# Kernel tuning notes

Measured on AMD Instinct MI355X. Metric: run time of the kernel, lower is better.

The kernel has to match this reference:

```python
import jax, jax.numpy as jnp
import numpy as np

N = 100000   # nodes
E = 1600000  # edges (avg degree 16)
D = 128      # in_dim == hidden
L = 3        # num_layers
G = 512      # graphs in batch


def setup_inputs() -> dict:
    key = jax.random.key(0)
    ks = jax.random.split(key, 14)
    s = 0.05
    return {
        "x": jax.random.normal(ks[0], (N, D), jnp.float32),
        "edge_index": jax.random.randint(ks[1], (2, E), 0, N, dtype=jnp.int32),
        "batch": jnp.sort(jax.random.randint(ks[2], (N,), 0, G, dtype=jnp.int32)),
        "W1": jax.random.normal(ks[3], (L, D, D), jnp.float32) * s,
        "b1": jax.random.normal(ks[4], (L, D), jnp.float32) * s,
        "W2": jax.random.normal(ks[5], (L, D, D), jnp.float32) * s,
        "b2": jax.random.normal(ks[6], (L, D), jnp.float32) * s,
        "gamma": jax.random.uniform(ks[7], (L, D), jnp.float32, 0.5, 1.5),
        "beta": jax.random.normal(ks[8], (L, D), jnp.float32) * s,
        "run_mean": jax.random.normal(ks[9], (L, D), jnp.float32) * s,
        "run_var": jax.random.uniform(ks[10], (L, D), jnp.float32, 0.5, 1.5),
        "eps": jnp.zeros((L,), jnp.float32),
        "lin1_W": jax.random.normal(ks[11], (D, D), jnp.float32) * s,
        "lin1_b": jax.random.normal(ks[12], (D,), jnp.float32) * s,
    }


def _bn(h, g, b, m, v):
    # BatchNorm1d in eval mode (running stats)
    return (h - m) * jax.lax.rsqrt(v + 1e-5) * g + b


def reference(x, edge_index, batch, W1, b1, W2, b2, gamma, beta,
              run_mean, run_var, eps, lin1_W, lin1_b):
    n = x.shape[0]
    src, dst = edge_index[0], edge_index[1]
    h = x
    for l in range(L):  # small fixed layer count
        # GINConv: sum-aggregate neighbor features then (1+eps)*self + agg
        agg = jax.ops.segment_sum(h[src], dst, num_segments=n)  # [N, D]
        z = (1.0 + eps[l]) * h + agg
        z = jax.nn.relu(z @ W1[l] + b1[l])
        z = jax.nn.relu(z @ W2[l] + b2[l])
        h = _bn(z, gamma[l], beta[l], run_mean[l], run_var[l])
    # global_mean_pool over graph ids
    counts = jax.ops.segment_sum(jnp.ones((n,), h.dtype), batch, num_segments=G)
    pooled = jax.ops.segment_sum(h, batch, num_segments=G)
    pooled = pooled / jnp.maximum(counts, 1.0)[:, None]  # [G, D]
    # lin1 + ReLU (dropout is identity in eval)
    return jax.nn.relu(pooled @ lin1_W + lin1_b)
```

## Files before the change

kernel.cpp:

```cpp
#include <hip/hip_runtime.h>
#include <hip/hip_bf16.h>

#define NN 100000
#define NE 1600000
#define DD 128
#define NL 3
#define NG 512
#define CSRP (NE + 8 * NN)
#define BSHIFT 9
#define NBUCK2 ((NN + 511) / 512)
#define ABLKS 512
#define ECHUNK (NE / ABLKS)

#define CONV_BLKS 12501
#define PREPW_BLKS 384
#define INIT_BLKS (CONV_BLKS + PREPW_BLKS + 1)

typedef __attribute__((ext_vector_type(8))) short bf16x8;
typedef __attribute__((ext_vector_type(4))) float f32x4;

__device__ __forceinline__ unsigned short f2bf(float f) {
    union { float f; unsigned int u; } x; x.f = f;
    unsigned int r = x.u + 0x7FFFu + ((x.u >> 16) & 1u);
    return (unsigned short)(r >> 16);
}
__device__ __forceinline__ float bf2f(unsigned short u) {
    union { unsigned int u; float f; } x; x.u = ((unsigned int)u) << 16;
    return x.f;
}
__device__ __forceinline__ float bflo(unsigned int v) { return bf2f((unsigned short)(v & 0xffffu)); }
__device__ __forceinline__ float bfhi(unsigned int v) { return bf2f((unsigned short)(v >> 16)); }
__device__ __forceinline__ unsigned cvtpk(float lo, float hi) {
    unsigned r;
    asm("v_cvt_pk_bf16_f32 %0, %1, %2" : "=v"(r) : "v"(lo), "v"(hi));
    return r;
}

__global__ __launch_bounds__(256) void init_all(const float* __restrict__ x,
                                                unsigned short* __restrict__ h0,
                                                unsigned short* __restrict__ h1,
                                                const float* __restrict__ W1,
                                                const float* __restrict__ W2,
                                                unsigned short* __restrict__ wbf,
                                                int* __restrict__ bcnt) {
    int bb = blockIdx.x;
    if (bb < CONV_BLKS) {
        long long t = (long long)bb * 256 + threadIdx.x;
        long long base = t * 4;
        if (base < (long long)NN * DD) {
            float4 v = *reinterpret_cast<const float4*>(x + base);
            ushort4 p;
            p.x = f2bf(v.x); p.y = f2bf(v.y); p.z = f2bf(v.z); p.w = f2bf(v.w);
            *reinterpret_cast<ushort4*>(h0 + base) = p;
        } else if (base < (long long)(NN + 1) * DD) {
            ushort4 z = {0, 0, 0, 0};
            *reinterpret_cast<ushort4*>(h0 + base) = z;
            *reinterpret_cast<ushort4*>(h1 + base) = z;
        }
        return;
    }
    bb -= CONV_BLKS;
    if (bb < PREPW_BLKS) {
        int idx = bb * 256 + threadIdx.x;
        int k = idx & 127;
        int n = (idx >> 7) & 127;
        int w = (idx >> 14) & 1;
        int l = idx >> 15;
        const float* src = w ? W2 : W1;
        wbf[idx] = f2bf(src[(l * DD + k) * DD + n]);
        return;
    }
    int i = threadIdx.x;
    if (i < NBUCK2) bcnt[i] = 0;
}

__global__ __launch_bounds__(256) void bcount(const int* __restrict__ ei,
                                              int* __restrict__ bcnt) {
    __shared__ int hist[NBUCK2];
    int tid = threadIdx.x;
    int e0 = blockIdx.x * ECHUNK;
    for (int i = tid; i < NBUCK2; i += 256) hist[i] = 0;
    __syncthreads();
    for (int i = tid; i < ECHUNK; i += 256)
        atomicAdd(&hist[ei[NE + e0 + i] >> BSHIFT], 1);
    __syncthreads();
    for (int i = tid; i < NBUCK2; i += 256) {
        int h = hist[i];
        if (h) atomicAdd(&bcnt[i], h);
    }
}

__global__ __launch_bounds__(256) void bscan(const int* __restrict__ bcnt,
                                             int* __restrict__ cboff,
                                             int* __restrict__ gpos) {
    __shared__ int s[256];
    int tid = threadIdx.x;
    int sum = (tid < NBUCK2) ? bcnt[tid] : 0;
    s[tid] = sum;
    __syncthreads();
    for (int o = 1; o < 256; o <<= 1) {
        int t = (tid >= o) ? s[tid - o] : 0;
        __syncthreads();
        s[tid] += t;
        __syncthreads();
    }
    if (tid < NBUCK2) {
        cboff[tid] = s[tid] - sum;
        gpos[tid] = 0;
    }
    if (tid == 0) cboff[NBUCK2] = NE;
}

__global__ __launch_bounds__(256) void binA(const int* __restrict__ ei,
                                            const int* __restrict__ cboff,
                                            int* __restrict__ gpos,
                                            int* __restrict__ ebuf) {
    __shared__ int hist[NBUCK2];
    __shared__ int sbase[NBUCK2];
    int tid = threadIdx.x;
    int e0 = blockIdx.x * ECHUNK;
    for (int i = tid; i < NBUCK2; i += 256) hist[i] = 0;
    __syncthreads();
    for (int i = tid; i < ECHUNK; i += 256) {
        int d = ei[NE + e0 + i];
        atomicAdd(&hist[d >> BSHIFT], 1);
    }
    __syncthreads();
    for (int i = tid; i < NBUCK2; i += 256) {
        int h = hist[i];
        sbase[i] = (h > 0) ? atomicAdd(&gpos[i], h) : 0;
        hist[i] = 0;
    }
    __syncthreads();
    for (int i = tid; i < ECHUNK; i += 256) {
        int s2 = ei[e0 + i];
        int d = ei[NE + e0 + i];
        int b = d >> BSHIFT;
        int pos = atomicAdd(&hist[b], 1);
        ebuf[cboff[b] + sbase[b] + pos] = s2 | ((d & 511) << 17);
    }
}

__global__ __launch_bounds__(256) void bpre(const int* __restrict__ ebuf,
                                            const int* __restrict__ cboff,
                                            int* __restrict__ rp,
                                            int* __restrict__ bsum) {
    __shared__ int lcnt[512];
    __shared__ int s[256];
    int b = blockIdx.x;
    int tid = threadIdx.x;
    lcnt[tid] = 0;
    lcnt[tid + 256] = 0;
    __syncthreads();
    int st = cboff[b], en = cboff[b + 1];
    for (int i = st + tid; i < en; i += 256)
        atomicAdd(&lcnt[ebuf[i] >> 17], 1);
    __syncthreads();
    int d0 = (lcnt[2 * tid] + 7) & ~7;
    int d1 = (lcnt[2 * tid + 1] + 7) & ~7;
    int ps = d0 + d1;
    s[tid] = ps;
    __syncthreads();
    for (int o = 1; o < 256; o <<= 1) {
        int t = (tid >= o) ? s[tid - o] : 0;
        __syncthreads();
        s[tid] += t;
        __syncthreads();
    }
    int base = s[tid] - ps;
    int node0 = (b << BSHIFT) + 2 * tid;
    if (node0 < NN) rp[node0] = base;
    if (node0 + 1 < NN) rp[node0 + 1] = base + d0;
    if (tid == 255) bsum[b] = s[255];
}

__global__ __launch_bounds__(256) void bscan2(const int* __restrict__ bsum,
                                              int* __restrict__ bbase,
                                              int* __restrict__ rp) {
    __shared__ int s[256];
    int tid = threadIdx.x;
    int sum = (tid < NBUCK2) ? bsum[tid] : 0;
    s[tid] = sum;
    __syncthreads();
    for (int o = 1; o < 256; o <<= 1) {
        int t = (tid >= o) ? s[tid - o] : 0;
        __syncthreads();
        s[tid] += t;
        __syncthreads();
    }
    if (tid < NBUCK2) bbase[tid] = s[tid] - sum;
    if (tid == 255) rp[NN] = s[255];
}

__global__ __launch_bounds__(256) void binB2(const int* __restrict__ ebuf,
                                             const int* __restrict__ cboff,
                                             const int* __restrict__ bbase,
                                             int* __restrict__ rp,
                                             int* __restrict__ csr) {
    __shared__ int rpl[512];
    __shared__ int lcnt[512];
    int b = blockIdx.x;
    int tid = threadIdx.x;
    int bb = bbase[b];
    for (int i = tid; i < 512; i += 256) {
        int node = (b << BSHIFT) + i;
        int v = 0;
        if (node < NN) {
            v = rp[node] + bb;
            rp[node] = v;
        }
        rpl[i] = v;
        lcnt[i] = 0;
    }
    __syncthreads();
    int st = cboff[b], en = cboff[b + 1];
    for (int i = st + tid; i < en; i += 256) {
        int v = ebuf[i];
        int dl = v >> 17;
        int pos = atomicAdd(&lcnt[dl], 1);
        csr[rpl[dl] + pos] = v & 0x1FFFF;
    }
    __syncthreads();
    for (int i = tid; i < 512; i += 256) {
        int node = (b << BSHIFT) + i;
        if (node >= NN) continue;
        int d = lcnt[i];
        int pd = (d + 7) & ~7;
        int base = rpl[i];
        for (int j = d; j < pd; ++j) csr[base + j] = NN;
    }
}

__global__ __launch_bounds__(256) void layer_fused(
    const unsigned short* __restrict__ hin,
    const int* __restrict__ rp,
    const int* __restrict__ csr,
    const unsigned short* __restrict__ w1t,
    const unsigned short* __restrict__ w2t,
    const float* __restrict__ b1,
    const float* __restrict__ b2,
    const float* __restrict__ gamma,
    const float* __restrict__ beta,
    const float* __restrict__ rmean,
    const float* __restrict__ rvar,
    const float* __restrict__ epsv,
    unsigned short* __restrict__ hout)
{
    __shared__ unsigned short z_lds[16 * 136];
    const int tid = threadIdx.x;
    const int lane = tid & 63;
    const int wave = tid >> 6;
    const int gid = lane >> 4;
    const int lg = lane & 15;
    const int row0 = blockIdx.x * 16;
    const float epl = 1.0f + epsv[0];
    const size_t lgo = (size_t)lg * 8;

#define ACC8(v) do { \
    acc[0] += bflo((v).x); acc[1] += bfhi((v).x); \
    acc[2] += bflo((v).y); acc[3] += bfhi((v).y); \
    acc[4] += bflo((v).z); acc[5] += bfhi((v).z); \
    acc[6] += bflo((v).w); acc[7] += bfhi((v).w); } while (0)

    const int rbase = row0 + (wave << 2);
    int pv = (lane < 5) ? rp[rbase + lane] : 0;
    const int st = __shfl(pv, gid);
    const int en = __shfl(pv, gid + 1);
    const int myrow = rbase + gid;

    float acc[8];
    {
        uint4 sv = *reinterpret_cast<const uint4*>(hin + (size_t)myrow * DD + lgo);
        acc[0] = epl * bflo(sv.x); acc[1] = epl * bfhi(sv.x);
        acc[2] = epl * bflo(sv.y); acc[3] = epl * bfhi(sv.y);
        acc[4] = epl * bflo(sv.z); acc[5] = epl * bfhi(sv.z);
        acc[6] = epl * bflo(sv.w); acc[7] = epl * bfhi(sv.w);
    }
    int c0 = st;
    for (; c0 + 16 <= en; c0 += 16) {
        int4 idA = *reinterpret_cast<const int4*>(csr + c0);
        int4 idB = *reinterpret_cast<const int4*>(csr + c0 + 4);
        int4 idC = *reinterpret_cast<const int4*>(csr + c0 + 8);
        int4 idD = *reinterpret_cast<const int4*>(csr + c0 + 12);
        uint4 v0 = *reinterpret_cast<const uint4*>(hin + (size_t)idA.x * DD + lgo);
        uint4 v1 = *reinterpret_cast<const uint4*>(hin + (size_t)idA.y * DD + lgo);
        uint4 v2 = *reinterpret_cast<const uint4*>(hin + (size_t)idA.z * DD + lgo);
        uint4 v3 = *reinterpret_cast<const uint4*>(hin + (size_t)idA.w * DD + lgo);
        uint4 v4 = *reinterpret_cast<const uint4*>(hin + (size_t)idB.x * DD + lgo);
        uint4 v5 = *reinterpret_cast<const uint4*>(hin + (size_t)idB.y * DD + lgo);
        uint4 v6 = *reinterpret_cast<const uint4*>(hin + (size_t)idB.z * DD + lgo);
        uint4 v7 = *reinterpret_cast<const uint4*>(hin + (size_t)idB.w * DD + lgo);
        uint4 v8 = *reinterpret_cast<const uint4*>(hin + (size_t)idC.x * DD + lgo);
        uint4 v9 = *reinterpret_cast<const uint4*>(hin + (size_t)idC.y * DD + lgo);
        uint4 va = *reinterpret_cast<const uint4*>(hin + (size_t)idC.z * DD + lgo);
        uint4 vb = *reinterpret_cast<const uint4*>(hin + (size_t)idC.w * DD + lgo);
        uint4 vc = *reinterpret_cast<const uint4*>(hin + (size_t)idD.x * DD + lgo);
        uint4 vd = *reinterpret_cast<const uint4*>(hin + (size_t)idD.y * DD + lgo);
        uint4 ve = *reinterpret_cast<const uint4*>(hin + (size_t)idD.z * DD + lgo);
        uint4 vf = *reinterpret_cast<const uint4*>(hin + (size_t)idD.w * DD + lgo);
        ACC8(v0); ACC8(v1); ACC8(v2); ACC8(v3);
        ACC8(v4); ACC8(v5); ACC8(v6); ACC8(v7);
        ACC8(v8); ACC8(v9); ACC8(va); ACC8(vb);
        ACC8(vc); ACC8(vd); ACC8(ve); ACC8(vf);
    }
    if (c0 < en) {
        int4 idA = *reinterpret_cast<const int4*>(csr + c0);
        int4 idB = *reinterpret_cast<const int4*>(csr + c0 + 4);
        uint4 v0 = *reinterpret_cast<const uint4*>(hin + (size_t)idA.x * DD + lgo);
        uint4 v1 = *reinterpret_cast<const uint4*>(hin + (size_t)idA.y * DD + lgo);
        uint4 v2 = *reinterpret_cast<const uint4*>(hin + (size_t)idA.z * DD + lgo);
        uint4 v3 = *reinterpret_cast<const uint4*>(hin + (size_t)idA.w * DD + lgo);
        uint4 v4 = *reinterpret_cast<const uint4*>(hin + (size_t)idB.x * DD + lgo);
        uint4 v5 = *reinterpret_cast<const uint4*>(hin + (size_t)idB.y * DD + lgo);
        uint4 v6 = *reinterpret_cast<const uint4*>(hin + (size_t)idB.z * DD + lgo);
        uint4 v7 = *reinterpret_cast<const uint4*>(hin + (size_t)idB.w * DD + lgo);
        ACC8(v0); ACC8(v1); ACC8(v2); ACC8(v3);
        ACC8(v4); ACC8(v5); ACC8(v6); ACC8(v7);
    }
    {
        uint4 pk;
        pk.x = cvtpk(acc[0], acc[1]);
        pk.y = cvtpk(acc[2], acc[3]);
        pk.z = cvtpk(acc[4], acc[5]);
        pk.w = cvtpk(acc[6], acc[7]);
        *reinterpret_cast<uint4*>(&z_lds[((wave << 2) + gid) * 136 + lg * 8]) = pk;
    }
    __syncthreads();

    const int l15 = lane & 15;
    const int kq = lane >> 4;
    const int colbase = wave << 5;

    bf16x8 afr[4];
    #pragma unroll
    for (int kk = 0; kk < 4; ++kk)
        afr[kk] = *reinterpret_cast<const bf16x8*>(&z_lds[l15 * 136 + kk * 32 + kq * 8]);
    __syncthreads();

    f32x4 acc4[2];
    #pragma unroll
    for (int nt = 0; nt < 2; ++nt) acc4[nt] = (f32x4){0.f, 0.f, 0.f, 0.f};
    #pragma unroll
    for (int nt = 0; nt < 2; ++nt) {
        #pragma unroll
        for (int kk = 0; kk < 4; ++kk) {
            bf16x8 bfr = *reinterpret_cast<const bf16x8*>(
                w1t + (colbase + nt * 16 + l15) * DD + kk * 32 + kq * 8);
            acc4[nt] = __builtin_amdgcn_mfma_f32_16x16x32_bf16(afr[kk], bfr, acc4[nt], 0, 0, 0);
        }
    }

    #pragma unroll
    for (int nt = 0; nt < 2; ++nt) {
        int col = colbase + nt * 16 + l15;
        float bv = b1[col];
        #pragma unroll
        for (int r = 0; r < 4; ++r) {
            int zr = kq * 4 + r;
            float v = acc4[nt][r] + bv;
            v = v > 0.f ? v : 0.f;
            z_lds[zr * 136 + col] = f2bf(v);
        }
    }
    __syncthreads();

    #pragma unroll
    for (int kk = 0; kk < 4; ++kk)
        afr[kk] = *reinterpret_cast<const bf16x8*>(&z_lds[l15 * 136 + kk * 32 + kq * 8]);
    #pragma unroll
    for (int nt = 0; nt < 2; ++nt) acc4[nt] = (f32x4){0.f, 0.f, 0.f, 0.f};
    #pragma unroll
    for (int nt = 0; nt < 2; ++nt) {
        #pragma unroll
        for (int kk = 0; kk < 4; ++kk) {
            bf16x8 bfr = *reinterpret_cast<const bf16x8*>(
                w2t + (colbase + nt * 16 + l15) * DD + kk * 32 + kq * 8);
            acc4[nt] = __builtin_amdgcn_mfma_f32_16x16x32_bf16(afr[kk], bfr, acc4[nt], 0, 0, 0);
        }
    }

    #pragma unroll
    for (int nt = 0; nt < 2; ++nt) {
        int col = colbase + nt * 16 + l15;
        float bv = b2[col];
        float ga = gamma[col];
        float be = beta[col];
        float mu = rmean[col];
        float inv = rsqrtf(rvar[col] + 1e-5f);
        #pragma unroll
        for (int r = 0; r < 4; ++r) {
            int zr = kq * 4 + r;
            float v = acc4[nt][r] + bv;
            v = v > 0.f ? v : 0.f;
            v = (v - mu) * inv * ga + be;
            hout[(size_t)(row0 + zr) * DD + col] = f2bf(v);
        }
    }
#undef ACC8
}

__global__ __launch_bounds__(256) void pool_final(const unsigned short* __restrict__ h,
                                                  const int* __restrict__ batch,
                                                  const float* __restrict__ W,
                                                  const float* __restrict__ b,
                                                  float* __restrict__ out) {
    int g = blockIdx.x;
    int t = threadIdx.x;
    int c2 = t & 63;
    int qu = t >> 6;

    int lo = 0, hi = NN;
    while (lo < hi) { int mid = (lo + hi) >> 1; if (batch[mid] < g) lo = mid + 1; else hi = mid; }
    int start = lo;
    hi = NN;
    while (lo < hi) { int mid = (lo + hi) >> 1; if (batch[mid] < g + 1) lo = mid + 1; else hi = mid; }
    int end = lo;

    float ax = 0.f, ay = 0.f;
    for (int i = start + qu; i < end; i += 4) {
        unsigned u = *reinterpret_cast<const unsigned*>(h + (size_t)i * DD + c2 * 2);
        ax += bflo(u); ay += bfhi(u);
    }

    __shared__ float ps[4][DD];
    ps[qu][c2 * 2] = ax;
    ps[qu][c2 * 2 + 1] = ay;
    __syncthreads();
    if (t < DD) {
        float inv = 1.0f / fmaxf((float)(end - start), 1.0f);
        ps[0][t] = (ps[0][t] + ps[1][t] + ps[2][t] + ps[3][t]) * inv;
    }
    __syncthreads();
    if (t < DD) {
        float o = b[t];
        #pragma unroll 8
        for (int k = 0; k < DD; ++k)
            o += ps[0][k] * W[k * DD + t];
        out[(size_t)g * DD + t] = fmaxf(o, 0.f);
    }
}

extern "C" void kernel_launch(void* const* d_in, const int* in_sizes, int n_in,
                              void* d_out, int out_size, void* d_ws, size_t ws_size,
                              hipStream_t stream) {
    const float* x     = (const float*)d_in[0];
    const int*   ei    = (const int*)d_in[1];
    const int*   batch = (const int*)d_in[2];
    const float* W1    = (const float*)d_in[3];
    const float* b1    = (const float*)d_in[4];
    const float* W2    = (const float*)d_in[5];
    const float* b2    = (const float*)d_in[6];
    const float* gamma = (const float*)d_in[7];
    const float* beta  = (const float*)d_in[8];
    const float* rmean = (const float*)d_in[9];
    const float* rvar  = (const float*)d_in[10];
    const float* eps   = (const float*)d_in[11];
    const float* lin1W = (const float*)d_in[12];
    const float* lin1b = (const float*)d_in[13];
    float* out = (float*)d_out;

    char* ws = (char*)d_ws;
    size_t off = 0;
    auto alloc = [&](size_t bytes) {
        void* p = ws + off;
        off = (off + bytes + 255) & ~(size_t)255;
        return p;
    };
    unsigned short* h0  = (unsigned short*)alloc((size_t)(NN + 1) * DD * 2);
    unsigned short* h1  = (unsigned short*)alloc((size_t)(NN + 1) * DD * 2);
    int* rp    = (int*)alloc((size_t)(NN + 1) * 4);
    int* bcnt  = (int*)alloc((size_t)NBUCK2 * 4);
    int* cboff = (int*)alloc((size_t)(NBUCK2 + 1) * 4);
    int* gpos  = (int*)alloc((size_t)NBUCK2 * 4);
    int* bsum  = (int*)alloc((size_t)NBUCK2 * 4);
    int* bbase = (int*)alloc((size_t)NBUCK2 * 4);
    int* csr   = (int*)alloc((size_t)CSRP * 4);
    int* ebuf  = (int*)alloc((size_t)NE * 4);
    unsigned short* wbf = (unsigned short*)alloc((size_t)NL * 2 * DD * DD * 2);

    init_all<<<INIT_BLKS, 256, 0, stream>>>(x, h0, h1, W1, W2, wbf, bcnt);

    bcount<<<ABLKS, 256, 0, stream>>>(ei, bcnt);
    bscan<<<1, 256, 0, stream>>>(bcnt, cboff, gpos);
    binA<<<ABLKS, 256, 0, stream>>>(ei, cboff, gpos, ebuf);
    bpre<<<NBUCK2, 256, 0, stream>>>(ebuf, cboff, rp, bsum);
    bscan2<<<1, 256, 0, stream>>>(bsum, bbase, rp);
    binB2<<<NBUCK2, 256, 0, stream>>>(ebuf, cboff, bbase, rp, csr);

    const int lgrid = NN / 16;
    layer_fused<<<lgrid, 256, 0, stream>>>(
        h0, rp, csr, wbf + 0 * DD * DD, wbf + 1 * DD * DD,
        b1 + 0 * DD, b2 + 0 * DD, gamma + 0 * DD, beta + 0 * DD,
        rmean + 0 * DD, rvar + 0 * DD, eps + 0, h1);
    layer_fused<<<lgrid, 256, 0, stream>>>(
        h1, rp, csr, wbf + 2 * DD * DD, wbf + 3 * DD * DD,
        b1 + 1 * DD, b2 + 1 * DD, gamma + 1 * DD, beta + 1 * DD,
        rmean + 1 * DD, rvar + 1 * DD, eps + 1, h0);
    layer_fused<<<lgrid, 256, 0, stream>>>(
        h0, rp, csr, wbf + 4 * DD * DD, wbf + 5 * DD * DD,
        b1 + 2 * DD, b2 + 2 * DD, gamma + 2 * DD, beta + 2 * DD,
        rmean + 2 * DD, rvar + 2 * DD, eps + 2, h1);

    pool_final<<<NG, 256, 0, stream>>>(h1, batch, lin1W, lin1b, out);
}
```

Baseline: 473.5 us.

## Sort nodes by padded degree to balance gather work across layer blocks

Builds a degree-binned permutation of nodes with four new small kernels: a histogram, a scan, a scatter and a job-table build. Each layer block then processes 16 nodes of similar degree, which reduces load imbalance between the lanes of a wave during neighbor aggregation. The gather loop is simplified to an 8-wide loop driven by a packed start/length job entry, and outputs are scattered back to the original row positions. The cost is extra preprocessing launches, indirect row writes and less locality between neighboring rows.

```diff
diff --git a/kernel.cpp b/kernel.cpp
--- a/kernel.cpp
+++ b/kernel.cpp
@@ -11,6 +11,7 @@
 #define NBUCK2 ((NN + 511) / 512)
 #define ABLKS 512
 #define ECHUNK (NE / ABLKS)
+#define NODE_BLKS ((NN + 255) / 256)
 
 #define CONV_BLKS 12501
 #define PREPW_BLKS 384
@@ -42,7 +43,8 @@
                                                 const float* __restrict__ W1,
                                                 const float* __restrict__ W2,
                                                 unsigned short* __restrict__ wbf,
-                                                int* __restrict__ bcnt) {
+                                                int* __restrict__ bcnt,
+                                                int* __restrict__ gdh) {
     int bb = blockIdx.x;
     if (bb < CONV_BLKS) {
         long long t = (long long)bb * 256 + threadIdx.x;
@@ -72,6 +74,7 @@
     }
     int i = threadIdx.x;
     if (i < NBUCK2) bcnt[i] = 0;
+    if (i < 64) gdh[i] = 0;
 }
 
 __global__ __launch_bounds__(256) void bcount(const int* __restrict__ ei,
@@ -196,7 +199,8 @@
                                              const int* __restrict__ cboff,
                                              const int* __restrict__ bbase,
                                              int* __restrict__ rp,
-                                             int* __restrict__ csr) {
+                                             int* __restrict__ csr,
+                                             int* __restrict__ degbin) {
     __shared__ int rpl[512];
     __shared__ int lcnt[512];
     int b = blockIdx.x;
@@ -228,12 +232,85 @@
         int pd = (d + 7) & ~7;
         int base = rpl[i];
         for (int j = d; j < pd; ++j) csr[base + j] = NN;
+        int bin = pd >> 3;
+        degbin[node] = bin < 63 ? bin : 63;
+    }
+}
+
+__global__ __launch_bounds__(256) void dcount(const int* __restrict__ degbin,
+                                              int* __restrict__ gdh) {
+    __shared__ int h[64];
+    int tid = threadIdx.x;
+    int i = blockIdx.x * 256 + tid;
+    if (tid < 64) h[tid] = 0;
+    __syncthreads();
+    if (i < NN) atomicAdd(&h[degbin[i]], 1);
+    __syncthreads();
+    if (tid < 64 && h[tid]) atomicAdd(&gdh[tid], h[tid]);
+}
+
+__global__ __launch_bounds__(256) void dscan(const int* __restrict__ gdh,
+                                             int* __restrict__ dbase,
+                                             int* __restrict__ dpos) {
+    __shared__ int s[64];
+    int tid = threadIdx.x;
+    if (tid < 64) s[tid] = gdh[tid];
+    __syncthreads();
+    for (int o = 1; o < 64; o <<= 1) {
+        int t = (tid >= o && tid < 64) ? s[tid - o] : 0;
+        __syncthreads();
+        if (tid < 64) s[tid] += t;
+        __syncthreads();
+    }
+    if (tid < 64) {
+        dbase[tid] = s[tid] - gdh[tid];
+        dpos[tid] = 0;
+    }
+}
+
+__global__ __launch_bounds__(256) void dperm(const int* __restrict__ degbin,
+                                             const int* __restrict__ dbase,
+                                             int* __restrict__ dpos,
+                                             int* __restrict__ perm) {
+    __shared__ int h[64];
+    __shared__ int sb[64];
+    int tid = threadIdx.x;
+    int i = blockIdx.x * 256 + tid;
+    int b = (i < NN) ? degbin[i] : -1;
+    if (tid < 64) h[tid] = 0;
+    __syncthreads();
+    if (b >= 0) atomicAdd(&h[b], 1);
+    __syncthreads();
+    if (tid < 64) {
+        int c = h[tid];
+        sb[tid] = c ? atomicAdd(&dpos[tid], c) : 0;
+        h[tid] = 0;
+    }
+    __syncthreads();
+    if (b >= 0) {
+        int p = atomicAdd(&h[b], 1);
+        perm[dbase[b] + sb[b] + p] = i;
+    }
+}
+
+__global__ __launch_bounds__(256) void jobbuild(const int* __restrict__ perm,
+                                                const int* __restrict__ rp,
+                                                int* __restrict__ job,
+                                                int* __restrict__ jnode) {
+    int i = blockIdx.x * 256 + threadIdx.x;
+    if (i < NN) {
+        int node = perm[i];
+        int st = rp[node];
+        int pd = rp[node + 1] - st;
+        job[i] = st | ((pd >> 3) << 22);
+        jnode[i] = node;
     }
 }
 
 __global__ __launch_bounds__(256) void layer_fused(
     const unsigned short* __restrict__ hin,
-    const int* __restrict__ rp,
+    const int* __restrict__ job,
+    const int* __restrict__ jnode,
     const int* __restrict__ csr,
     const unsigned short* __restrict__ w1t,
     const unsigned short* __restrict__ w2t,
@@ -247,6 +324,7 @@
     unsigned short* __restrict__ hout)
 {
     __shared__ unsigned short z_lds[16 * 136];
+    __shared__ int jrow[16];
     const int tid = threadIdx.x;
     const int lane = tid & 63;
     const int wave = tid >> 6;
@@ -262,11 +340,13 @@
     acc[4] += bflo((v).z); acc[5] += bfhi((v).z); \
     acc[6] += bflo((v).w); acc[7] += bfhi((v).w); } while (0)
 
-    const int rbase = row0 + (wave << 2);
-    int pv = (lane < 5) ? rp[rbase + lane] : 0;
-    const int st = __shfl(pv, gid);
-    const int en = __shfl(pv, gid + 1);
-    const int myrow = rbase + gid;
+    if (tid < 16) jrow[tid] = jnode[row0 + tid];
+
+    const int idx = row0 + (wave << 2) + gid;
+    const int jb = job[idx];
+    const int myrow = jnode[idx];
+    const int st = jb & 0x3FFFFF;
+    const int en = st + ((jb >> 22) << 3);
 
     float acc[8];
     {
@@ -276,34 +356,7 @@
         acc[4] = epl * bflo(sv.z); acc[5] = epl * bfhi(sv.z);
         acc[6] = epl * bflo(sv.w); acc[7] = epl * bfhi(sv.w);
     }
-    int c0 = st;
-    for (; c0 + 16 <= en; c0 += 16) {
-        int4 idA = *reinterpret_cast<const int4*>(csr + c0);
-        int4 idB = *reinterpret_cast<const int4*>(csr + c0 + 4);
-        int4 idC = *reinterpret_cast<const int4*>(csr + c0 + 8);
-        int4 idD = *reinterpret_cast<const int4*>(csr + c0 + 12);
-        uint4 v0 = *reinterpret_cast<const uint4*>(hin + (size_t)idA.x * DD + lgo);
-        uint4 v1 = *reinterpret_cast<const uint4*>(hin + (size_t)idA.y * DD + lgo);
-        uint4 v2 = *reinterpret_cast<const uint4*>(hin + (size_t)idA.z * DD + lgo);
-        uint4 v3 = *reinterpret_cast<const uint4*>(hin + (size_t)idA.w * DD + lgo);
-        uint4 v4 = *reinterpret_cast<const uint4*>(hin + (size_t)idB.x * DD + lgo);
-        uint4 v5 = *reinterpret_cast<const uint4*>(hin + (size_t)idB.y * DD + lgo);
-        uint4 v6 = *reinterpret_cast<const uint4*>(hin + (size_t)idB.z * DD + lgo);
-        uint4 v7 = *reinterpret_cast<const uint4*>(hin + (size_t)idB.w * DD + lgo);
-        uint4 v8 = *reinterpret_cast<const uint4*>(hin + (size_t)idC.x * DD + lgo);
-        uint4 v9 = *reinterpret_cast<const uint4*>(hin + (size_t)idC.y * DD + lgo);
-        uint4 va = *reinterpret_cast<const uint4*>(hin + (size_t)idC.z * DD + lgo);
-        uint4 vb = *reinterpret_cast<const uint4*>(hin + (size_t)idC.w * DD + lgo);
-        uint4 vc = *reinterpret_cast<const uint4*>(hin + (size_t)idD.x * DD + lgo);
-        uint4 vd = *reinterpret_cast<const uint4*>(hin + (size_t)idD.y * DD + lgo);
-        uint4 ve = *reinterpret_cast<const uint4*>(hin + (size_t)idD.z * DD + lgo);
-        uint4 vf = *reinterpret_cast<const uint4*>(hin + (size_t)idD.w * DD + lgo);
-        ACC8(v0); ACC8(v1); ACC8(v2); ACC8(v3);
-        ACC8(v4); ACC8(v5); ACC8(v6); ACC8(v7);
-        ACC8(v8); ACC8(v9); ACC8(va); ACC8(vb);
-        ACC8(vc); ACC8(vd); ACC8(ve); ACC8(vf);
-    }
-    if (c0 < en) {
+    for (int c0 = st; c0 < en; c0 += 8) {
         int4 idA = *reinterpret_cast<const int4*>(csr + c0);
         int4 idB = *reinterpret_cast<const int4*>(csr + c0 + 4);
         uint4 v0 = *reinterpret_cast<const uint4*>(hin + (size_t)idA.x * DD + lgo);
@@ -390,10 +443,11 @@
         #pragma unroll
         for (int r = 0; r < 4; ++r) {
             int zr = kq * 4 + r;
+            int gr = jrow[zr];
             float v = acc4[nt][r] + bv;
             v = v > 0.f ? v : 0.f;
             v = (v - mu) * inv * ga + be;
-            hout[(size_t)(row0 + zr) * DD + col] = f2bf(v);
+            hout[(size_t)gr * DD + col] = f2bf(v);
         }
     }
 #undef ACC8
@@ -468,36 +522,48 @@
     };
     unsigned short* h0  = (unsigned short*)alloc((size_t)(NN + 1) * DD * 2);
     unsigned short* h1  = (unsigned short*)alloc((size_t)(NN + 1) * DD * 2);
-    int* rp    = (int*)alloc((size_t)(NN + 1) * 4);
-    int* bcnt  = (int*)alloc((size_t)NBUCK2 * 4);
-    int* cboff = (int*)alloc((size_t)(NBUCK2 + 1) * 4);
-    int* gpos  = (int*)alloc((size_t)NBUCK2 * 4);
-    int* bsum  = (int*)alloc((size_t)NBUCK2 * 4);
-    int* bbase = (int*)alloc((size_t)NBUCK2 * 4);
-    int* csr   = (int*)alloc((size_t)CSRP * 4);
-    int* ebuf  = (int*)alloc((size_t)NE * 4);
+    int* rp     = (int*)alloc((size_t)(NN + 1) * 4);
+    int* bcnt   = (int*)alloc((size_t)NBUCK2 * 4);
+    int* cboff  = (int*)alloc((size_t)(NBUCK2 + 1) * 4);
+    int* gpos   = (int*)alloc((size_t)NBUCK2 * 4);
+    int* bsum   = (int*)alloc((size_t)NBUCK2 * 4);
+    int* bbase  = (int*)alloc((size_t)NBUCK2 * 4);
+    int* csr    = (int*)alloc((size_t)CSRP * 4);
+    int* ebuf   = (int*)alloc((size_t)NE * 4);
+    int* degbin = (int*)alloc((size_t)NN * 4);
+    int* gdh    = (int*)alloc(64 * 4);
+    int* dbase  = (int*)alloc(64 * 4);
+    int* dpos   = (int*)alloc(64 * 4);
+    int* perm   = (int*)alloc((size_t)NN * 4);
+    int* job    = (int*)alloc((size_t)NN * 4);
+    int* jnode  = (int*)alloc((size_t)NN * 4);
     unsigned short* wbf = (unsigned short*)alloc((size_t)NL * 2 * DD * DD * 2);
 
-    init_all<<<INIT_BLKS, 256, 0, stream>>>(x, h0, h1, W1, W2, wbf, bcnt);
+    init_all<<<INIT_BLKS, 256, 0, stream>>>(x, h0, h1, W1, W2, wbf, bcnt, gdh);
 
     bcount<<<ABLKS, 256, 0, stream>>>(ei, bcnt);
     bscan<<<1, 256, 0, stream>>>(bcnt, cboff, gpos);
     binA<<<ABLKS, 256, 0, stream>>>(ei, cboff, gpos, ebuf);
     bpre<<<NBUCK2, 256, 0, stream>>>(ebuf, cboff, rp, bsum);
     bscan2<<<1, 256, 0, stream>>>(bsum, bbase, rp);
-    binB2<<<NBUCK2, 256, 0, stream>>>(ebuf, cboff, bbase, rp, csr);
+    binB2<<<NBUCK2, 256, 0, stream>>>(ebuf, cboff, bbase, rp, csr, degbin);
+
+    dcount<<<NODE_BLKS, 256, 0, stream>>>(degbin, gdh);
+    dscan<<<1, 256, 0, stream>>>(gdh, dbase, dpos);
+    dperm<<<NODE_BLKS, 256, 0, stream>>>(degbin, dbase, dpos, perm);
+    jobbuild<<<NODE_BLKS, 256, 0, stream>>>(perm, rp, job, jnode);
 
     const int lgrid = NN / 16;
     layer_fused<<<lgrid, 256, 0, stream>>>(
-        h0, rp, csr, wbf + 0 * DD * DD, wbf + 1 * DD * DD,
+        h0, job, jnode, csr, wbf + 0 * DD * DD, wbf + 1 * DD * DD,
         b1 + 0 * DD, b2 + 0 * DD, gamma + 0 * DD, beta + 0 * DD,
         rmean + 0 * DD, rvar + 0 * DD, eps + 0, h1);
     layer_fused<<<lgrid, 256, 0, stream>>>(
-        h1, rp, csr, wbf + 2 * DD * DD, wbf + 3 * DD * DD,
+        h1, job, jnode, csr, wbf + 2 * DD * DD, wbf + 3 * DD * DD,
         b1 + 1 * DD, b2 + 1 * DD, gamma + 1 * DD, beta + 1 * DD,
         rmean + 1 * DD, rvar + 1 * DD, eps + 1, h0);
     layer_fused<<<lgrid, 256, 0, stream>>>(
-        h0, rp, csr, wbf + 4 * DD * DD, wbf + 5 * DD * DD,
+        h0, job, jnode, csr, wbf + 4 * DD * DD, wbf + 5 * DD * DD,
         b1 + 2 * DD, b2 + 2 * DD, gamma + 2 * DD, beta + 2 * DD,
         rmean + 2 * DD, rvar + 2 * DD, eps + 2, h1);
 
```

Result: no change. 478.4 us (+1.0%).

## Merge CSR build kernels into one cooperative kernel with grid syncs

Applied to the files above, without the earlier changes.

Replaces the seven preprocessing kernels (init, bucket count, scan, bin, prefix, scan, scatter) with a single cooperative kernel of 1024 blocks that separates the phases with grid.sync. The goal is to remove per-launch gaps and tail effects between the small dependent kernels. It also simplifies the gather loop in the layer kernel from a 16-wide unroll to an 8-wide loop, which shortens the code but lowers memory-level parallelism. Grid syncs add their own cost, and phases that use only one block leave the rest of the grid idle.

```diff
diff --git a/kernel.cpp b/kernel.cpp
--- a/kernel.cpp
+++ b/kernel.cpp
@@ -1,5 +1,8 @@
 #include <hip/hip_runtime.h>
 #include <hip/hip_bf16.h>
+#include <hip/hip_cooperative_groups.h>
+
+namespace cg = cooperative_groups;
 
 #define NN 100000
 #define NE 1600000
@@ -11,10 +14,8 @@
 #define NBUCK2 ((NN + 511) / 512)
 #define ABLKS 512
 #define ECHUNK (NE / ABLKS)
-
-#define CONV_BLKS 12501
-#define PREPW_BLKS 384
-#define INIT_BLKS (CONV_BLKS + PREPW_BLKS + 1)
+#define COOP_BLKS 1024
+#define GSTRIDE (COOP_BLKS * 256)
 
 typedef __attribute__((ext_vector_type(8))) short bf16x8;
 typedef __attribute__((ext_vector_type(4))) float f32x4;
@@ -36,198 +37,191 @@
     return r;
 }
 
-__global__ __launch_bounds__(256) void init_all(const float* __restrict__ x,
-                                                unsigned short* __restrict__ h0,
-                                                unsigned short* __restrict__ h1,
-                                                const float* __restrict__ W1,
-                                                const float* __restrict__ W2,
-                                                unsigned short* __restrict__ wbf,
-                                                int* __restrict__ bcnt) {
-    int bb = blockIdx.x;
-    if (bb < CONV_BLKS) {
-        long long t = (long long)bb * 256 + threadIdx.x;
-        long long base = t * 4;
-        if (base < (long long)NN * DD) {
-            float4 v = *reinterpret_cast<const float4*>(x + base);
-            ushort4 p;
-            p.x = f2bf(v.x); p.y = f2bf(v.y); p.z = f2bf(v.z); p.w = f2bf(v.w);
-            *reinterpret_cast<ushort4*>(h0 + base) = p;
-        } else if (base < (long long)(NN + 1) * DD) {
-            ushort4 z = {0, 0, 0, 0};
-            *reinterpret_cast<ushort4*>(h0 + base) = z;
-            *reinterpret_cast<ushort4*>(h1 + base) = z;
-        }
-        return;
-    }
-    bb -= CONV_BLKS;
-    if (bb < PREPW_BLKS) {
-        int idx = bb * 256 + threadIdx.x;
-        int k = idx & 127;
-        int n = (idx >> 7) & 127;
-        int w = (idx >> 14) & 1;
-        int l = idx >> 15;
-        const float* src = w ? W2 : W1;
-        wbf[idx] = f2bf(src[(l * DD + k) * DD + n]);
-        return;
-    }
-    int i = threadIdx.x;
-    if (i < NBUCK2) bcnt[i] = 0;
-}
-
-__global__ __launch_bounds__(256) void bcount(const int* __restrict__ ei,
-                                              int* __restrict__ bcnt) {
-    __shared__ int hist[NBUCK2];
-    int tid = threadIdx.x;
-    int e0 = blockIdx.x * ECHUNK;
-    for (int i = tid; i < NBUCK2; i += 256) hist[i] = 0;
-    __syncthreads();
-    for (int i = tid; i < ECHUNK; i += 256)
-        atomicAdd(&hist[ei[NE + e0 + i] >> BSHIFT], 1);
-    __syncthreads();
-    for (int i = tid; i < NBUCK2; i += 256) {
-        int h = hist[i];
-        if (h) atomicAdd(&bcnt[i], h);
-    }
-}
-
-__global__ __launch_bounds__(256) void bscan(const int* __restrict__ bcnt,
-                                             int* __restrict__ cboff,
-                                             int* __restrict__ gpos) {
-    __shared__ int s[256];
-    int tid = threadIdx.x;
-    int sum = (tid < NBUCK2) ? bcnt[tid] : 0;
-    s[tid] = sum;
-    __syncthreads();
-    for (int o = 1; o < 256; o <<= 1) {
-        int t = (tid >= o) ? s[tid - o] : 0;
-        __syncthreads();
-        s[tid] += t;
-        __syncthreads();
-    }
-    if (tid < NBUCK2) {
-        cboff[tid] = s[tid] - sum;
-        gpos[tid] = 0;
-    }
-    if (tid == 0) cboff[NBUCK2] = NE;
-}
-
-__global__ __launch_bounds__(256) void binA(const int* __restrict__ ei,
-                                            const int* __restrict__ cboff,
-                                            int* __restrict__ gpos,
-                                            int* __restrict__ ebuf) {
-    __shared__ int hist[NBUCK2];
-    __shared__ int sbase[NBUCK2];
-    int tid = threadIdx.x;
-    int e0 = blockIdx.x * ECHUNK;
-    for (int i = tid; i < NBUCK2; i += 256) hist[i] = 0;
-    __syncthreads();
-    for (int i = tid; i < ECHUNK; i += 256) {
-        int d = ei[NE + e0 + i];
-        atomicAdd(&hist[d >> BSHIFT], 1);
-    }
-    __syncthreads();
-    for (int i = tid; i < NBUCK2; i += 256) {
-        int h = hist[i];
-        sbase[i] = (h > 0) ? atomicAdd(&gpos[i], h) : 0;
-        hist[i] = 0;
-    }
-    __syncthreads();
-    for (int i = tid; i < ECHUNK; i += 256) {
-        int s2 = ei[e0 + i];
-        int d = ei[NE + e0 + i];
-        int b = d >> BSHIFT;
-        int pos = atomicAdd(&hist[b], 1);
-        ebuf[cboff[b] + sbase[b] + pos] = s2 | ((d & 511) << 17);
-    }
-}
-
-__global__ __launch_bounds__(256) void bpre(const int* __restrict__ ebuf,
-                                            const int* __restrict__ cboff,
-                                            int* __restrict__ rp,
-                                            int* __restrict__ bsum) {
-    __shared__ int lcnt[512];
-    __shared__ int s[256];
-    int b = blockIdx.x;
-    int tid = threadIdx.x;
-    lcnt[tid] = 0;
-    lcnt[tid + 256] = 0;
-    __syncthreads();
-    int st = cboff[b], en = cboff[b + 1];
-    for (int i = st + tid; i < en; i += 256)
-        atomicAdd(&lcnt[ebuf[i] >> 17], 1);
-    __syncthreads();
-    int d0 = (lcnt[2 * tid] + 7) & ~7;
-    int d1 = (lcnt[2 * tid + 1] + 7) & ~7;
-    int ps = d0 + d1;
-    s[tid] = ps;
-    __syncthreads();
-    for (int o = 1; o < 256; o <<= 1) {
-        int t = (tid >= o) ? s[tid - o] : 0;
-        __syncthreads();
-        s[tid] += t;
-        __syncthreads();
-    }
-    int base = s[tid] - ps;
-    int node0 = (b << BSHIFT) + 2 * tid;
-    if (node0 < NN) rp[node0] = base;
-    if (node0 + 1 < NN) rp[node0 + 1] = base + d0;
-    if (tid == 255) bsum[b] = s[255];
-}
-
-__global__ __launch_bounds__(256) void bscan2(const int* __restrict__ bsum,
-                                              int* __restrict__ bbase,
-                                              int* __restrict__ rp) {
-    __shared__ int s[256];
-    int tid = threadIdx.x;
-    int sum = (tid < NBUCK2) ? bsum[tid] : 0;
-    s[tid] = sum;
-    __syncthreads();
-    for (int o = 1; o < 256; o <<= 1) {
-        int t = (tid >= o) ? s[tid - o] : 0;
-        __syncthreads();
-        s[tid] += t;
-        __syncthreads();
-    }
-    if (tid < NBUCK2) bbase[tid] = s[tid] - sum;
-    if (tid == 255) rp[NN] = s[255];
-}
-
-__global__ __launch_bounds__(256) void binB2(const int* __restrict__ ebuf,
-                                             const int* __restrict__ cboff,
-                                             const int* __restrict__ bbase,
-                                             int* __restrict__ rp,
-                                             int* __restrict__ csr) {
-    __shared__ int rpl[512];
-    __shared__ int lcnt[512];
-    int b = blockIdx.x;
-    int tid = threadIdx.x;
-    int bb = bbase[b];
-    for (int i = tid; i < 512; i += 256) {
-        int node = (b << BSHIFT) + i;
-        int v = 0;
-        if (node < NN) {
-            v = rp[node] + bb;
-            rp[node] = v;
-        }
-        rpl[i] = v;
-        lcnt[i] = 0;
-    }
-    __syncthreads();
-    int st = cboff[b], en = cboff[b + 1];
-    for (int i = st + tid; i < en; i += 256) {
-        int v = ebuf[i];
-        int dl = v >> 17;
-        int pos = atomicAdd(&lcnt[dl], 1);
-        csr[rpl[dl] + pos] = v & 0x1FFFF;
-    }
-    __syncthreads();
-    for (int i = tid; i < 512; i += 256) {
-        int node = (b << BSHIFT) + i;
-        if (node >= NN) continue;
-        int d = lcnt[i];
-        int pd = (d + 7) & ~7;
-        int base = rpl[i];
-        for (int j = d; j < pd; ++j) csr[base + j] = NN;
+__global__ __launch_bounds__(256) void build_all(
+    const float* __restrict__ x,
+    unsigned short* __restrict__ h0,
+    unsigned short* __restrict__ h1,
+    const float* __restrict__ W1,
+    const float* __restrict__ W2,
+    unsigned short* __restrict__ wbf,
+    const int* __restrict__ ei,
+    int* __restrict__ bcnt,
+    int* __restrict__ cboff,
+    int* __restrict__ gpos,
+    int* __restrict__ ebuf,
+    int* __restrict__ rp,
+    int* __restrict__ bsum,
+    int* __restrict__ bbase,
+    int* __restrict__ csr)
+{
+    cg::grid_group grid = cg::this_grid();
+    __shared__ int smem[1024];
+    const int tid = threadIdx.x;
+    const int bid = blockIdx.x;
+    const int gthread = bid * 256 + tid;
+
+    {
+        const long long tot = (long long)(NN + 1) * DD / 4;
+        for (long long t = gthread; t < tot; t += GSTRIDE) {
+            long long base = t * 4;
+            if (base < (long long)NN * DD) {
+                float4 v = *reinterpret_cast<const float4*>(x + base);
+                ushort4 p;
+                p.x = f2bf(v.x); p.y = f2bf(v.y); p.z = f2bf(v.z); p.w = f2bf(v.w);
+                *reinterpret_cast<ushort4*>(h0 + base) = p;
+            } else {
+                ushort4 z = {0, 0, 0, 0};
+                *reinterpret_cast<ushort4*>(h0 + base) = z;
+                *reinterpret_cast<ushort4*>(h1 + base) = z;
+            }
+        }
+        for (int i = gthread; i < NL * 2 * DD * DD; i += GSTRIDE) {
+            int k = i & 127;
+            int n = (i >> 7) & 127;
+            int w = (i >> 14) & 1;
+            int l = i >> 15;
+            const float* src = w ? W2 : W1;
+            wbf[i] = f2bf(src[(l * DD + k) * DD + n]);
+        }
+        if (gthread < NBUCK2) bcnt[gthread] = 0;
+    }
+    grid.sync();
+
+    if (bid < ABLKS) {
+        int* hist = smem;
+        for (int i = tid; i < NBUCK2; i += 256) hist[i] = 0;
+        __syncthreads();
+        int e0 = bid * ECHUNK;
+        for (int i = tid; i < ECHUNK; i += 256)
+            atomicAdd(&hist[ei[NE + e0 + i] >> BSHIFT], 1);
+        __syncthreads();
+        for (int i = tid; i < NBUCK2; i += 256) {
+            int h = hist[i];
+            if (h) atomicAdd(&bcnt[i], h);
+        }
+    }
+    grid.sync();
+
+    if (bid == 0) {
+        int* s = smem;
+        int sum = (tid < NBUCK2) ? bcnt[tid] : 0;
+        s[tid] = sum;
+        __syncthreads();
+        for (int o = 1; o < 256; o <<= 1) {
+            int t2 = (tid >= o) ? s[tid - o] : 0;
+            __syncthreads();
+            s[tid] += t2;
+            __syncthreads();
+        }
+        if (tid < NBUCK2) {
+            cboff[tid] = s[tid] - sum;
+            gpos[tid] = 0;
+        }
+        if (tid == 0) cboff[NBUCK2] = NE;
+    }
+    grid.sync();
+
+    if (bid < ABLKS) {
+        int* hist = smem;
+        int* sbase = smem + 256;
+        for (int i = tid; i < NBUCK2; i += 256) hist[i] = 0;
+        __syncthreads();
+        int e0 = bid * ECHUNK;
+        for (int i = tid; i < ECHUNK; i += 256)
+            atomicAdd(&hist[ei[NE + e0 + i] >> BSHIFT], 1);
+        __syncthreads();
+        for (int i = tid; i < NBUCK2; i += 256) {
+            int h = hist[i];
+            sbase[i] = (h > 0) ? atomicAdd(&gpos[i], h) : 0;
+            hist[i] = 0;
+        }
+        __syncthreads();
+        for (int i = tid; i < ECHUNK; i += 256) {
+            int s2 = ei[e0 + i];
+            int d = ei[NE + e0 + i];
+            int b = d >> BSHIFT;
+            int pos = atomicAdd(&hist[b], 1);
+            ebuf[cboff[b] + sbase[b] + pos] = s2 | ((d & 511) << 17);
+        }
+    }
+    grid.sync();
+
+    if (bid < NBUCK2) {
+        int* lcnt = smem;
+        int* s = smem + 512;
+        lcnt[tid] = 0;
+        lcnt[tid + 256] = 0;
+        __syncthreads();
+        int st = cboff[bid], en = cboff[bid + 1];
+        for (int i = st + tid; i < en; i += 256)
+            atomicAdd(&lcnt[ebuf[i] >> 17], 1);
+        __syncthreads();
+        int d0 = (lcnt[2 * tid] + 7) & ~7;
+        int d1 = (lcnt[2 * tid + 1] + 7) & ~7;
+        int ps = d0 + d1;
+        s[tid] = ps;
+        __syncthreads();
+        for (int o = 1; o < 256; o <<= 1) {
+            int t2 = (tid >= o) ? s[tid - o] : 0;
+            __syncthreads();
+            s[tid] += t2;
+            __syncthreads();
+        }
+        int base = s[tid] - ps;
+        int node0 = (bid << BSHIFT) + 2 * tid;
+        if (node0 < NN) rp[node0] = base;
+        if (node0 + 1 < NN) rp[node0 + 1] = base + d0;
+        if (tid == 255) bsum[bid] = s[255];
+    }
+    grid.sync();
+
+    if (bid == 0) {
+        int* s = smem;
+        int sum = (tid < NBUCK2) ? bsum[tid] : 0;
+        s[tid] = sum;
+        __syncthreads();
+        for (int o = 1; o < 256; o <<= 1) {
+            int t2 = (tid >= o) ? s[tid - o] : 0;
+            __syncthreads();
+            s[tid] += t2;
+            __syncthreads();
+        }
+        if (tid < NBUCK2) bbase[tid] = s[tid] - sum;
+        if (tid == 255) rp[NN] = s[255];
+    }
+    grid.sync();
+
+    if (bid < NBUCK2) {
+        int* rpl = smem;
+        int* lcnt = smem + 512;
+        int bb = bbase[bid];
+        for (int i = tid; i < 512; i += 256) {
+            int node = (bid << BSHIFT) + i;
+            int v = 0;
+            if (node < NN) {
+                v = rp[node] + bb;
+                rp[node] = v;
+            }
+            rpl[i] = v;
+            lcnt[i] = 0;
+        }
+        __syncthreads();
+        int st = cboff[bid], en = cboff[bid + 1];
+        for (int i = st + tid; i < en; i += 256) {
+            int v = ebuf[i];
+            int dl = v >> 17;
+            int pos = atomicAdd(&lcnt[dl], 1);
+            csr[rpl[dl] + pos] = v & 0x1FFFF;
+        }
+        __syncthreads();
+        for (int i = tid; i < 512; i += 256) {
+            int node = (bid << BSHIFT) + i;
+            if (node >= NN) continue;
+            int d = lcnt[i];
+            int pd = (d + 7) & ~7;
+            int base = rpl[i];
+            for (int j = d; j < pd; ++j) csr[base + j] = NN;
+        }
     }
 }
 
@@ -276,34 +270,7 @@
         acc[4] = epl * bflo(sv.z); acc[5] = epl * bfhi(sv.z);
         acc[6] = epl * bflo(sv.w); acc[7] = epl * bfhi(sv.w);
     }
-    int c0 = st;
-    for (; c0 + 16 <= en; c0 += 16) {
-        int4 idA = *reinterpret_cast<const int4*>(csr + c0);
-        int4 idB = *reinterpret_cast<const int4*>(csr + c0 + 4);
-        int4 idC = *reinterpret_cast<const int4*>(csr + c0 + 8);
-        int4 idD = *reinterpret_cast<const int4*>(csr + c0 + 12);
-        uint4 v0 = *reinterpret_cast<const uint4*>(hin + (size_t)idA.x * DD + lgo);
-        uint4 v1 = *reinterpret_cast<const uint4*>(hin + (size_t)idA.y * DD + lgo);
-        uint4 v2 = *reinterpret_cast<const uint4*>(hin + (size_t)idA.z * DD + lgo);
-        uint4 v3 = *reinterpret_cast<const uint4*>(hin + (size_t)idA.w * DD + lgo);
-        uint4 v4 = *reinterpret_cast<const uint4*>(hin + (size_t)idB.x * DD + lgo);
-        uint4 v5 = *reinterpret_cast<const uint4*>(hin + (size_t)idB.y * DD + lgo);
-        uint4 v6 = *reinterpret_cast<const uint4*>(hin + (size_t)idB.z * DD + lgo);
-        uint4 v7 = *reinterpret_cast<const uint4*>(hin + (size_t)idB.w * DD + lgo);
-        uint4 v8 = *reinterpret_cast<const uint4*>(hin + (size_t)idC.x * DD + lgo);
-        uint4 v9 = *reinterpret_cast<const uint4*>(hin + (size_t)idC.y * DD + lgo);
-        uint4 va = *reinterpret_cast<const uint4*>(hin + (size_t)idC.z * DD + lgo);
-        uint4 vb = *reinterpret_cast<const uint4*>(hin + (size_t)idC.w * DD + lgo);
-        uint4 vc = *reinterpret_cast<const uint4*>(hin + (size_t)idD.x * DD + lgo);
-        uint4 vd = *reinterpret_cast<const uint4*>(hin + (size_t)idD.y * DD + lgo);
-        uint4 ve = *reinterpret_cast<const uint4*>(hin + (size_t)idD.z * DD + lgo);
-        uint4 vf = *reinterpret_cast<const uint4*>(hin + (size_t)idD.w * DD + lgo);
-        ACC8(v0); ACC8(v1); ACC8(v2); ACC8(v3);
-        ACC8(v4); ACC8(v5); ACC8(v6); ACC8(v7);
-        ACC8(v8); ACC8(v9); ACC8(va); ACC8(vb);
-        ACC8(vc); ACC8(vd); ACC8(ve); ACC8(vf);
-    }
-    if (c0 < en) {
+    for (int c0 = st; c0 < en; c0 += 8) {
         int4 idA = *reinterpret_cast<const int4*>(csr + c0);
         int4 idB = *reinterpret_cast<const int4*>(csr + c0 + 4);
         uint4 v0 = *reinterpret_cast<const uint4*>(hin + (size_t)idA.x * DD + lgo);
@@ -468,24 +435,25 @@
     };
     unsigned short* h0  = (unsigned short*)alloc((size_t)(NN + 1) * DD * 2);
     unsigned short* h1  = (unsigned short*)alloc((size_t)(NN + 1) * DD * 2);
-    int* rp    = (int*)alloc((size_t)(NN + 1) * 4);
-    int* bcnt  = (int*)alloc((size_t)NBUCK2 * 4);
-    int* cboff = (int*)alloc((size_t)(NBUCK2 + 1) * 4);
-    int* gpos  = (int*)alloc((size_t)NBUCK2 * 4);
-    int* bsum  = (int*)alloc((size_t)NBUCK2 * 4);
-    int* bbase = (int*)alloc((size_t)NBUCK2 * 4);
-    int* csr   = (int*)alloc((size_t)CSRP * 4);
-    int* ebuf  = (int*)alloc((size_t)NE * 4);
+    int* rp     = (int*)alloc((size_t)(NN + 1) * 4);
+    int* bcnt   = (int*)alloc((size_t)NBUCK2 * 4);
+    int* cboff  = (int*)alloc((size_t)(NBUCK2 + 1) * 4);
+    int* gpos   = (int*)alloc((size_t)NBUCK2 * 4);
+    int* bsum   = (int*)alloc((size_t)NBUCK2 * 4);
+    int* bbase  = (int*)alloc((size_t)NBUCK2 * 4);
+    int* csr    = (int*)alloc((size_t)CSRP * 4);
+    int* ebuf   = (int*)alloc((size_t)NE * 4);
     unsigned short* wbf = (unsigned short*)alloc((size_t)NL * 2 * DD * DD * 2);
 
-    init_all<<<INIT_BLKS, 256, 0, stream>>>(x, h0, h1, W1, W2, wbf, bcnt);
-
-    bcount<<<ABLKS, 256, 0, stream>>>(ei, bcnt);
-    bscan<<<1, 256, 0, stream>>>(bcnt, cboff, gpos);
-    binA<<<ABLKS, 256, 0, stream>>>(ei, cboff, gpos, ebuf);
-    bpre<<<NBUCK2, 256, 0, stream>>>(ebuf, cboff, rp, bsum);
-    bscan2<<<1, 256, 0, stream>>>(bsum, bbase, rp);
-    binB2<<<NBUCK2, 256, 0, stream>>>(ebuf, cboff, bbase, rp, csr);
+    {
+        void* args[] = {
+            (void*)&x, (void*)&h0, (void*)&h1, (void*)&W1, (void*)&W2, (void*)&wbf,
+            (void*)&ei, (void*)&bcnt, (void*)&cboff, (void*)&gpos, (void*)&ebuf,
+            (void*)&rp, (void*)&bsum, (void*)&bbase, (void*)&csr
+        };
+        hipLaunchCooperativeKernel((void*)build_all, dim3(COOP_BLKS), dim3(256),
+                                   args, 0, stream);
+    }
 
     const int lgrid = NN / 16;
     layer_fused<<<lgrid, 256, 0, stream>>>(
```

New measurement: 1.118 ms. +136.1%, slower.
